# Performance work log

Measured on AMD Instinct MI355X. Metric: run time of the kernel, lower is better.

Reference implementation:

```python
import jax, jax.numpy as jnp
import numpy as np

C = 1024  # in_channels
B, SQ, SKV = 4, 2048, 2048


def setup_inputs() -> dict:
    key = jax.random.key(0)
    ks = jax.random.split(key, 10)
    s = 1.0 / np.sqrt(C)
    return {
        "x": jax.random.normal(ks[0], (B, SQ, C), jnp.float32),
        "content_embeddings": jax.random.normal(ks[1], (B, SKV, C), jnp.float32),
        "Wq": jax.random.normal(ks[2], (C, C), jnp.float32) * s,
        "bq": jnp.zeros((C,), jnp.float32),
        "Wk": jax.random.normal(ks[3], (C, C), jnp.float32) * s,
        "bk": jnp.zeros((C,), jnp.float32),
        "Wv": jax.random.normal(ks[4], (C, C), jnp.float32) * s,
        "bv": jnp.zeros((C,), jnp.float32),
        "Wo": jax.random.normal(ks[5], (C, C), jnp.float32) * s,
        "bo": jnp.zeros((C,), jnp.float32),
    }


def reference(x, content_embeddings, Wq, bq, Wk, bk, Wv, bv, Wo, bo):
    # torch Linear: y = x @ W.T + b
    queries = x @ Wq.T + bq                    # [B, SQ, C]
    keys = content_embeddings @ Wk.T + bk      # [B, SKV, C]
    values = content_embeddings @ Wv.T + bv    # [B, SKV, C]
    scale = 1.0 / jnp.sqrt(jnp.asarray(C, x.dtype))
    scores = jnp.einsum("bqc,bkc->bqk", queries, keys) * scale  # [B, SQ, SKV]
    attn = jax.nn.softmax(scores, axis=-1)
    attended = jnp.einsum("bqk,bkc->bqc", attn, values)         # [B, SQ, C]
    out = x + attended
    return out @ Wo.T + bo
```

## Files before the change

kernel.cpp:

```cpp
#include <hip/hip_runtime.h>


typedef __attribute__((ext_vector_type(8))) short short8;
typedef __attribute__((ext_vector_type(8))) unsigned short ushort8;
typedef __attribute__((ext_vector_type(4))) unsigned short ushort4v;
typedef __attribute__((ext_vector_type(4))) float f32x4;

__device__ __forceinline__ float b2f(unsigned short u) {
  union { unsigned int i; float f; } x;
  x.i = ((unsigned int)u) << 16;
  return x.f;
}
__device__ __forceinline__ unsigned short f2b(float f) {
  union { float f; unsigned int i; } x;
  x.f = f;
  unsigned int i = x.i;
  i += 0x7fffu + ((i >> 16) & 1u);
  return (unsigned short)(i >> 16);
}

__device__ __forceinline__ void async_copy16(const void* g, void* l) {
  __builtin_amdgcn_global_load_lds(
      (const __attribute__((address_space(1))) unsigned int*)g,
      (__attribute__((address_space(3))) unsigned int*)l, 16, 0, 0);
}

__global__ void detect_fmt(const unsigned short* __restrict__ x, int* flag) {
  __shared__ int cnt;
  if (threadIdx.x == 0) cnt = 0;
  __syncthreads();
  int c = 0;
  for (int i = threadIdx.x * 2; i < 8192; i += 512) {
    unsigned e = (x[i] >> 7) & 0xFF;
    if (e >= 0x90) ++c;
  }
  atomicAdd(&cnt, c);
  __syncthreads();
  if (threadIdx.x == 0) *flag = (cnt > 64) ? 1 : 0;
}

struct CvtArgs { const void* src[10]; };

__global__ __launch_bounds__(256) void convert_all(
    CvtArgs a, unsigned short* __restrict__ dst, const int* __restrict__ flag) {
  const bool f32 = (*flag != 0);
  const long nchunk = 2621952;
  for (long c = blockIdx.x * 256L + threadIdx.x; c < nchunk;
       c += 1024L * 256) {
    const long flat = c * 8;
    int t; long off;
    if      (flat < 8388608)  { t = 0; off = 0; }
    else if (flat < 16777216) { t = 1; off = 8388608; }
    else if (flat < 17825792) { t = 2; off = 16777216; }
    else if (flat < 17826816) { t = 3; off = 17825792; }
    else if (flat < 18875392) { t = 4; off = 17826816; }
    else if (flat < 18876416) { t = 5; off = 18875392; }
    else if (flat < 19924992) { t = 6; off = 18876416; }
    else if (flat < 19926016) { t = 7; off = 19924992; }
    else if (flat < 20974592) { t = 8; off = 19926016; }
    else                      { t = 9; off = 20974592; }
    const long li = flat - off;
    if (f32) {
      const float* s = (const float*)a.src[t] + li;
      const f32x4 lo = *(const f32x4*)s;
      const f32x4 hi = *(const f32x4*)(s + 4);
      ushort8 o;
      o[0] = f2b(lo[0]); o[1] = f2b(lo[1]); o[2] = f2b(lo[2]); o[3] = f2b(lo[3]);
      o[4] = f2b(hi[0]); o[5] = f2b(hi[1]); o[6] = f2b(hi[2]); o[7] = f2b(hi[3]);
      *(ushort8*)(dst + flat) = o;
    } else {
      *(ushort8*)(dst + flat) =
          *(const ushort8*)((const unsigned short*)a.src[t] + li);
    }
  }
}

#define MODE_BIAS 0
#define MODE_RES  2
#define MODE_SB   3
#define MODE_OUT  4

__device__ __forceinline__ void xcd_swizzle(int gx, int gy, int& bx, int& by) {
  const int L = blockIdx.y * gx + blockIdx.x;
  const int r = L & 7, m = L >> 3;
  bx = m % gx;
  by = r * (gy >> 3) + m / gx;
}

template <int MODE, int KU>
__device__ __forceinline__ void gemm_core(
    const unsigned short* __restrict__ A, const unsigned short* __restrict__ B,
    void* __restrict__ C, const unsigned short* __restrict__ bias,
    const unsigned short* __restrict__ Res, const int* __restrict__ flg,
    int N, int K, float scale, int bx, int by, int vt) {
  __shared__ __align__(16) unsigned short As[KU * 128 * 32];
  __shared__ __align__(16) unsigned short Bs[KU * 128 * 32];
  const int tid = threadIdx.x;
  const int wave = tid >> 6, lane = tid & 63;
  const int wm = wave >> 1, wn = wave & 1;
  const int quad = lane >> 4, lrow = lane & 15;

  const long arow0 = (long)by * 128 + (tid >> 2);
  const long brow0 = (long)bx * 128 + (tid >> 2);
  const int cstg = (tid & 3) * 8;
  const unsigned short* ag0 = A + arow0 * K + cstg;
  const unsigned short* ag1 = ag0 + 64L * K;
  const unsigned short* bg0 = B + brow0 * K + cstg;
  const unsigned short* bg1 = bg0 + 64L * K;
  char* lA0 = (char*)As + tid * 16;
  char* lA1 = (char*)As + (256 + tid) * 16;
  char* lB0 = (char*)Bs + tid * 16;
  char* lB1 = (char*)Bs + (256 + tid) * 16;

  f32x4 acc[4][4];
#pragma unroll
  for (int i = 0; i < 4; ++i)
#pragma unroll
    for (int j = 0; j < 4; ++j) acc[i][j] = (f32x4){0.f, 0.f, 0.f, 0.f};

  for (int kt = 0; kt < K; kt += 32 * KU) {
#pragma unroll
    for (int u = 0; u < KU; ++u) {
      async_copy16(ag0 + kt + u * 32, lA0 + u * 8192);
      async_copy16(ag1 + kt + u * 32, lA1 + u * 8192);
      async_copy16(bg0 + kt + u * 32, lB0 + u * 8192);
      async_copy16(bg1 + kt + u * 32, lB1 + u * 8192);
    }
    __syncthreads();
#pragma unroll
    for (int u = 0; u < KU; ++u) {
      const unsigned short* Au = As + u * 4096;
      const unsigned short* Bu = Bs + u * 4096;
      short8 af[4], bfr[4];
#pragma unroll
      for (int i = 0; i < 4; ++i)
        af[i] = *(const short8*)(Au + (wm * 64 + i * 16 + lrow) * 32 + quad * 8);
#pragma unroll
      for (int j = 0; j < 4; ++j)
        bfr[j] =
            *(const short8*)(Bu + (wn * 64 + j * 16 + lrow) * 32 + quad * 8);
#pragma unroll
      for (int i = 0; i < 4; ++i)
#pragma unroll
        for (int j = 0; j < 4; ++j)
          acc[i][j] = __builtin_amdgcn_mfma_f32_16x16x32_bf16(
              af[i], bfr[j], acc[i][j], 0, 0, 0);
    }
    __syncthreads();
  }

  const bool f32out = (MODE == MODE_OUT) ? (*flg != 0) : false;
#pragma unroll
  for (int i = 0; i < 4; ++i) {
    const long row = (long)by * 128 + wm * 64 + i * 16 + quad * 4;
#pragma unroll
    for (int j = 0; j < 4; ++j) {
      const long col = (long)bx * 128 + wn * 64 + j * 16 + lrow;
      if (MODE == MODE_BIAS && vt) {
        const float bb = b2f(bias[col]);
        ushort4v pk;
#pragma unroll
        for (int r = 0; r < 4; ++r) pk[r] = f2b(acc[i][j][r] + bb);
        const long b = row >> 11, kvr = row & 2047;
        *(ushort4v*)((unsigned short*)C + b * 2097152 + col * 2048 + kvr) = pk;
        continue;
      }
#pragma unroll
      for (int r = 0; r < 4; ++r) {
        const float v = acc[i][j][r];
        const long idx = (row + r) * N + col;
        if (MODE == MODE_BIAS) {
          ((unsigned short*)C)[idx] = f2b(v + b2f(bias[col]));
        } else if (MODE == MODE_SB) {
          ((unsigned short*)C)[idx] = f2b(v * scale);
        } else if (MODE == MODE_RES) {
          ((unsigned short*)C)[idx] = f2b(v + b2f(Res[idx]));
        } else {
          const float o = v + b2f(bias[col]);
          if (f32out) ((float*)C)[idx] = o;
          else        ((unsigned short*)C)[idx] = f2b(o);
        }
      }
    }
  }
}

template <int MODE, int KU>
__global__ __launch_bounds__(256, 2) void gemm_nt(
    const unsigned short* __restrict__ A, const unsigned short* __restrict__ B,
    void* __restrict__ C, const unsigned short* __restrict__ bias,
    const unsigned short* __restrict__ Res, const int* __restrict__ flg,
    int N, int K, float scale, long sA, long sB, long sC, long sR) {
  const int bz = blockIdx.z;
  int bx, by;
  xcd_swizzle(gridDim.x, gridDim.y, bx, by);
  const unsigned short* Rb = (MODE == MODE_RES) ? Res + bz * sR : nullptr;
  void* Cb = (MODE == MODE_OUT) ? (void*)((char*)C)
                                : (void*)((unsigned short*)C + bz * sC);
  gemm_core<MODE, KU>(A + bz * sA, B + bz * sB, Cb, bias, Rb, flg, N, K, scale,
                      bx, by, 0);
}

struct QkvArgs {
  const unsigned short* A[3];
  const unsigned short* B[3];
  unsigned short* C[3];
  const unsigned short* bias[3];
};
__global__ __launch_bounds__(256, 2) void gemm_qkv(QkvArgs a, int N, int K) {
  const int z = blockIdx.z;
  int bx, by;
  xcd_swizzle(gridDim.x, gridDim.y, bx, by);
  gemm_core<MODE_BIAS, 2>(a.A[z], a.B[z], a.C[z], a.bias[z], nullptr, nullptr,
                          N, K, 1.f, bx, by, z == 2 ? 1 : 0);
}

__global__ __launch_bounds__(256) void softmax_rows(
    unsigned short* __restrict__ SP) {
  unsigned short* s = SP + blockIdx.x * 2048L;
  const int tid = threadIdx.x;
  const ushort8 raw = *(const ushort8*)(s + tid * 8);
  float v[8];
#pragma unroll
  for (int i = 0; i < 8; ++i) v[i] = b2f(raw[i]);
  float m = v[0];
#pragma unroll
  for (int i = 1; i < 8; ++i) m = fmaxf(m, v[i]);
#pragma unroll
  for (int off = 32; off > 0; off >>= 1) m = fmaxf(m, __shfl_xor(m, off));
  __shared__ float redm[4], reds[4];
  if ((tid & 63) == 0) redm[tid >> 6] = m;
  __syncthreads();
  m = fmaxf(fmaxf(redm[0], redm[1]), fmaxf(redm[2], redm[3]));
  float sum = 0.f;
#pragma unroll
  for (int i = 0; i < 8; ++i) {
    v[i] = __expf(v[i] - m);
    sum += v[i];
  }
#pragma unroll
  for (int off = 32; off > 0; off >>= 1) sum += __shfl_xor(sum, off);
  if ((tid & 63) == 0) reds[tid >> 6] = sum;
  __syncthreads();
  sum = reds[0] + reds[1] + reds[2] + reds[3];
  const float inv = 1.0f / sum;
  ushort8 o;
#pragma unroll
  for (int i = 0; i < 8; ++i) o[i] = f2b(v[i] * inv);
  *(ushort8*)(s + tid * 8) = o;
}

extern "C" void kernel_launch(void* const* d_in, const int* in_sizes, int n_in,
                              void* d_out, int out_size, void* d_ws,
                              size_t ws_size, hipStream_t stream) {
  char* ws = (char*)d_ws;
  const long MB = 1 << 20;
  unsigned short* C0  = (unsigned short*)ws;
  unsigned short* xb  = C0;
  unsigned short* ceb = C0 + 8388608;
  unsigned short* Wqb = C0 + 16777216;
  unsigned short* bqb = C0 + 17825792;
  unsigned short* Wkb = C0 + 17826816;
  unsigned short* bkb = C0 + 18875392;
  unsigned short* Wvb = C0 + 18876416;
  unsigned short* bvb = C0 + 19924992;
  unsigned short* Wob = C0 + 19926016;
  unsigned short* bob = C0 + 20974592;
  int*            flg = (int*)(ws + 41 * MB);
  unsigned short* Q   = (unsigned short*)(ws + 42 * MB);
  unsigned short* Kp  = (unsigned short*)(ws + 58 * MB);
  unsigned short* Vt  = (unsigned short*)(ws + 74 * MB);
  unsigned short* S   = (unsigned short*)(ws + 90 * MB);
  unsigned short* Ar  = Kp;

  const dim3 blk(256);
  const float scale = 0.03125f;

  detect_fmt<<<dim3(1), dim3(256), 0, stream>>>((const unsigned short*)d_in[0],
                                                flg);
  CvtArgs ca;
  for (int i = 0; i < 10; ++i) ca.src[i] = d_in[i];
  convert_all<<<dim3(1024), blk, 0, stream>>>(ca, C0, flg);

  QkvArgs qa;
  qa.A[0] = xb;  qa.A[1] = ceb; qa.A[2] = ceb;
  qa.B[0] = Wqb; qa.B[1] = Wkb; qa.B[2] = Wvb;
  qa.C[0] = Q;   qa.C[1] = Kp;  qa.C[2] = Vt;
  qa.bias[0] = bqb; qa.bias[1] = bkb; qa.bias[2] = bvb;
  gemm_qkv<<<dim3(8, 64, 3), blk, 0, stream>>>(qa, 1024, 1024);

  gemm_nt<MODE_SB, 2><<<dim3(16, 16, 4), blk, 0, stream>>>(
      Q, Kp, S, nullptr, nullptr, nullptr, 2048, 1024, scale,
      2048L * 1024, 2048L * 1024, 2048L * 2048, 0);

  softmax_rows<<<dim3(8192), blk, 0, stream>>>(S);

  gemm_nt<MODE_RES, 2><<<dim3(8, 16, 4), blk, 0, stream>>>(
      S, Vt, Ar, nullptr, xb, nullptr, 1024, 2048, 1.f,
      2048L * 2048, 1024L * 2048, 2048L * 1024, 2048L * 1024);

  gemm_nt<MODE_OUT, 2><<<dim3(8, 64, 1), blk, 0, stream>>>(
      Ar, Wob, d_out, bob, nullptr, flg, 1024, 1024, 1.f, 0, 0, 0, 0);
}
```

Measured before the change: 323.2 us.

## Add 256x256-tile 8-wave GEMM core for QKV projection and QK^T scores

```diff
diff --git a/kernel.cpp b/kernel.cpp
--- a/kernel.cpp
+++ b/kernel.cpp
@@ -201,17 +201,218 @@
                       bx, by, 0);
 }
 
+template <int MODE>
+__device__ __forceinline__ void gemm256_core(
+    const unsigned short* __restrict__ A, const unsigned short* __restrict__ B,
+    void* __restrict__ C, const unsigned short* __restrict__ bias,
+    const unsigned short* __restrict__ Res, const int* __restrict__ flg,
+    int N, int K, float scale, int bx, int by, int vt) {
+  __shared__ __align__(16) unsigned short lds[65536];
+  const int tid = threadIdx.x;
+  const int wave = tid >> 6, lane = tid & 63;
+  const int wm = wave >> 2, wn = wave & 3;
+  const int quad = lane >> 4, lrow = lane & 15;
+  const int NT = K >> 6;
+
+  const int srow = tid >> 3;
+  const int sch = (tid & 7) ^ (srow & 7);
+  const unsigned short* gA = A + (long)(by * 256 + srow) * K + sch * 8;
+  const unsigned short* gB = B + (long)(bx * 256 + srow) * K + sch * 8;
+  char* const ldst = (char*)lds + tid * 16;
+
+  auto stageA = [&](int ts, int h) {
+    const unsigned short* g = gA + (long)h * 128 * K + ts * 64;
+    char* l = ldst + (ts & 1) * 32768 + h * 16384;
+    async_copy16(g, l);
+    async_copy16(g + (long)64 * K, l + 8192);
+  };
+  auto stageB = [&](int ts, int h) {
+    const unsigned short* g = gB + (long)h * 128 * K + ts * 64;
+    char* l = ldst + 65536 + (ts & 1) * 32768 + h * 16384;
+    async_copy16(g, l);
+    async_copy16(g + (long)64 * K, l + 8192);
+  };
+
+  const int chk0 = ((quad) ^ (lrow & 7)) << 3;
+  const int chk1 = ((4 + quad) ^ (lrow & 7)) << 3;
+
+  f32x4 acc[8][4];
+#pragma unroll
+  for (int i = 0; i < 8; ++i)
+#pragma unroll
+    for (int j = 0; j < 4; ++j) acc[i][j] = (f32x4){0.f, 0.f, 0.f, 0.f};
+
+  stageB(0, 0); stageB(0, 1); stageA(0, 0); stageA(0, 1);
+  stageB(1, 0); stageB(1, 1);
+  asm volatile("s_waitcnt vmcnt(4)" ::: "memory");
+  __builtin_amdgcn_s_barrier();
+
+  for (int t = 0; t < NT; ++t) {
+    const unsigned short* Au = lds + (t & 1) * 16384 + (wm * 128 + lrow) * 64;
+    const unsigned short* Bu =
+        lds + 32768 + (t & 1) * 16384 + (wn * 64 + lrow) * 64;
+    short8 a[4][2], blo[2][2], bhi[2][2];
+
+#pragma unroll
+    for (int i = 0; i < 4; ++i) {
+      a[i][0] = *(const short8*)(Au + i * 1024 + chk0);
+      a[i][1] = *(const short8*)(Au + i * 1024 + chk1);
+    }
+#pragma unroll
+    for (int j = 0; j < 2; ++j) {
+      blo[j][0] = *(const short8*)(Bu + j * 1024 + chk0);
+      blo[j][1] = *(const short8*)(Bu + j * 1024 + chk1);
+    }
+    if (t + 1 < NT) stageA(t + 1, 0);
+    __builtin_amdgcn_s_barrier();
+    asm volatile("s_waitcnt lgkmcnt(0)" ::: "memory");
+    __builtin_amdgcn_sched_barrier(0);
+    __builtin_amdgcn_s_setprio(1);
+#pragma unroll
+    for (int i = 0; i < 4; ++i)
+#pragma unroll
+      for (int j = 0; j < 2; ++j) {
+        acc[i][j] = __builtin_amdgcn_mfma_f32_16x16x32_bf16(
+            a[i][0], blo[j][0], acc[i][j], 0, 0, 0);
+        acc[i][j] = __builtin_amdgcn_mfma_f32_16x16x32_bf16(
+            a[i][1], blo[j][1], acc[i][j], 0, 0, 0);
+      }
+    __builtin_amdgcn_s_setprio(0);
+    __builtin_amdgcn_s_barrier();
+
+#pragma unroll
+    for (int j = 0; j < 2; ++j) {
+      bhi[j][0] = *(const short8*)(Bu + (j + 2) * 1024 + chk0);
+      bhi[j][1] = *(const short8*)(Bu + (j + 2) * 1024 + chk1);
+    }
+    if (t + 1 < NT) stageA(t + 1, 1);
+    __builtin_amdgcn_s_barrier();
+    asm volatile("s_waitcnt lgkmcnt(0)" ::: "memory");
+    __builtin_amdgcn_sched_barrier(0);
+    __builtin_amdgcn_s_setprio(1);
+#pragma unroll
+    for (int i = 0; i < 4; ++i)
+#pragma unroll
+      for (int j = 0; j < 2; ++j) {
+        acc[i][j + 2] = __builtin_amdgcn_mfma_f32_16x16x32_bf16(
+            a[i][0], bhi[j][0], acc[i][j + 2], 0, 0, 0);
+        acc[i][j + 2] = __builtin_amdgcn_mfma_f32_16x16x32_bf16(
+            a[i][1], bhi[j][1], acc[i][j + 2], 0, 0, 0);
+      }
+    __builtin_amdgcn_s_setprio(0);
+    __builtin_amdgcn_s_barrier();
+
+#pragma unroll
+    for (int i = 0; i < 4; ++i) {
+      a[i][0] = *(const short8*)(Au + (i + 4) * 1024 + chk0);
+      a[i][1] = *(const short8*)(Au + (i + 4) * 1024 + chk1);
+    }
+    if (t + 2 < NT) stageB(t + 2, 0);
+    __builtin_amdgcn_s_barrier();
+    asm volatile("s_waitcnt lgkmcnt(0)" ::: "memory");
+    __builtin_amdgcn_sched_barrier(0);
+    __builtin_amdgcn_s_setprio(1);
+#pragma unroll
+    for (int i = 0; i < 4; ++i)
+#pragma unroll
+      for (int j = 0; j < 2; ++j) {
+        acc[i + 4][j + 2] = __builtin_amdgcn_mfma_f32_16x16x32_bf16(
+            a[i][0], bhi[j][0], acc[i + 4][j + 2], 0, 0, 0);
+        acc[i + 4][j + 2] = __builtin_amdgcn_mfma_f32_16x16x32_bf16(
+            a[i][1], bhi[j][1], acc[i + 4][j + 2], 0, 0, 0);
+      }
+    __builtin_amdgcn_s_setprio(0);
+    __builtin_amdgcn_s_barrier();
+
+    if (t + 2 < NT) stageB(t + 2, 1);
+    __builtin_amdgcn_s_barrier();
+    __builtin_amdgcn_s_setprio(1);
+#pragma unroll
+    for (int i = 0; i < 4; ++i)
+#pragma unroll
+      for (int j = 0; j < 2; ++j) {
+        acc[i + 4][j] = __builtin_amdgcn_mfma_f32_16x16x32_bf16(
+            a[i][0], blo[j][0], acc[i + 4][j], 0, 0, 0);
+        acc[i + 4][j] = __builtin_amdgcn_mfma_f32_16x16x32_bf16(
+            a[i][1], blo[j][1], acc[i + 4][j], 0, 0, 0);
+      }
+    __builtin_amdgcn_s_setprio(0);
+    if (t + 2 < NT) {
+      asm volatile("s_waitcnt vmcnt(4)" ::: "memory");
+    } else {
+      asm volatile("s_waitcnt vmcnt(0)" ::: "memory");
+    }
+    __builtin_amdgcn_s_barrier();
+  }
+
+  const bool f32out = (MODE == MODE_OUT) ? (*flg != 0) : false;
+  float bb[4];
+  if (MODE == MODE_BIAS || MODE == MODE_OUT) {
+#pragma unroll
+    for (int j = 0; j < 4; ++j)
+      bb[j] = b2f(bias[(long)bx * 256 + wn * 64 + j * 16 + lrow]);
+  }
+#pragma unroll
+  for (int i = 0; i < 8; ++i) {
+    const long row = (long)by * 256 + wm * 128 + i * 16 + quad * 4;
+#pragma unroll
+    for (int j = 0; j < 4; ++j) {
+      const long col = (long)bx * 256 + wn * 64 + j * 16 + lrow;
+      if (MODE == MODE_BIAS && vt) {
+        ushort4v pk;
+#pragma unroll
+        for (int r = 0; r < 4; ++r) pk[r] = f2b(acc[i][j][r] + bb[j]);
+        const long b = row >> 11, kvr = row & 2047;
+        *(ushort4v*)((unsigned short*)C + b * 2097152 + col * 2048 + kvr) = pk;
+        continue;
+      }
+#pragma unroll
+      for (int r = 0; r < 4; ++r) {
+        const float v = acc[i][j][r];
+        const long idx = (row + r) * N + col;
+        if (MODE == MODE_BIAS) {
+          ((unsigned short*)C)[idx] = f2b(v + bb[j]);
+        } else if (MODE == MODE_SB) {
+          ((unsigned short*)C)[idx] = f2b(v * scale);
+        } else if (MODE == MODE_RES) {
+          ((unsigned short*)C)[idx] = f2b(v + b2f(Res[idx]));
+        } else {
+          const float o = v + bb[j];
+          if (f32out) ((float*)C)[idx] = o;
+          else        ((unsigned short*)C)[idx] = f2b(o);
+        }
+      }
+    }
+  }
+}
+
+template <int MODE>
+__global__ __launch_bounds__(512, 2) void gemm_nt256(
+    const unsigned short* __restrict__ A, const unsigned short* __restrict__ B,
+    void* __restrict__ C, const unsigned short* __restrict__ bias,
+    const unsigned short* __restrict__ Res, const int* __restrict__ flg,
+    int N, int K, float scale, long sA, long sB, long sC, long sR) {
+  const int bz = blockIdx.z;
+  int bx, by;
+  xcd_swizzle(gridDim.x, gridDim.y, bx, by);
+  const unsigned short* Rb = (MODE == MODE_RES) ? Res + bz * sR : nullptr;
+  void* Cb = (MODE == MODE_OUT) ? (void*)((char*)C)
+                                : (void*)((unsigned short*)C + bz * sC);
+  gemm256_core<MODE>(A + bz * sA, B + bz * sB, Cb, bias, Rb, flg, N, K, scale,
+                     bx, by, 0);
+}
+
 struct QkvArgs {
   const unsigned short* A[3];
   const unsigned short* B[3];
   unsigned short* C[3];
   const unsigned short* bias[3];
 };
-__global__ __launch_bounds__(256, 2) void gemm_qkv(QkvArgs a, int N, int K) {
+__global__ __launch_bounds__(512, 2) void gemm_qkv(QkvArgs a, int N, int K) {
   const int z = blockIdx.z;
   int bx, by;
   xcd_swizzle(gridDim.x, gridDim.y, bx, by);
-  gemm_core<MODE_BIAS, 2>(a.A[z], a.B[z], a.C[z], a.bias[z], nullptr, nullptr,
+  gemm256_core<MODE_BIAS>(a.A[z], a.B[z], a.C[z], a.bias[z], nullptr, nullptr,
                           N, K, 1.f, bx, by, z == 2 ? 1 : 0);
 }
 
@@ -273,32 +474,31 @@
   unsigned short* S   = (unsigned short*)(ws + 90 * MB);
   unsigned short* Ar  = Kp;
 
-  const dim3 blk(256);
   const float scale = 0.03125f;
 
   detect_fmt<<<dim3(1), dim3(256), 0, stream>>>((const unsigned short*)d_in[0],
                                                 flg);
   CvtArgs ca;
   for (int i = 0; i < 10; ++i) ca.src[i] = d_in[i];
-  convert_all<<<dim3(1024), blk, 0, stream>>>(ca, C0, flg);
+  convert_all<<<dim3(1024), dim3(256), 0, stream>>>(ca, C0, flg);
 
   QkvArgs qa;
   qa.A[0] = xb;  qa.A[1] = ceb; qa.A[2] = ceb;
   qa.B[0] = Wqb; qa.B[1] = Wkb; qa.B[2] = Wvb;
   qa.C[0] = Q;   qa.C[1] = Kp;  qa.C[2] = Vt;
   qa.bias[0] = bqb; qa.bias[1] = bkb; qa.bias[2] = bvb;
-  gemm_qkv<<<dim3(8, 64, 3), blk, 0, stream>>>(qa, 1024, 1024);
-
-  gemm_nt<MODE_SB, 2><<<dim3(16, 16, 4), blk, 0, stream>>>(
+  gemm_qkv<<<dim3(4, 32, 3), dim3(512), 0, stream>>>(qa, 1024, 1024);
+
+  gemm_nt256<MODE_SB><<<dim3(8, 8, 4), dim3(512), 0, stream>>>(
       Q, Kp, S, nullptr, nullptr, nullptr, 2048, 1024, scale,
       2048L * 1024, 2048L * 1024, 2048L * 2048, 0);
 
-  softmax_rows<<<dim3(8192), blk, 0, stream>>>(S);
-
-  gemm_nt<MODE_RES, 2><<<dim3(8, 16, 4), blk, 0, stream>>>(
+  softmax_rows<<<dim3(8192), dim3(256), 0, stream>>>(S);
+
+  gemm_nt<MODE_RES, 2><<<dim3(8, 16, 4), dim3(256), 0, stream>>>(
       S, Vt, Ar, nullptr, xb, nullptr, 1024, 2048, 1.f,
       2048L * 2048, 1024L * 2048, 2048L * 1024, 2048L * 1024);
 
-  gemm_nt<MODE_OUT, 2><<<dim3(8, 64, 1), blk, 0, stream>>>(
+  gemm_nt<MODE_OUT, 2><<<dim3(8, 64, 1), dim3(256), 0, stream>>>(
       Ar, Wob, d_out, bob, nullptr, flg, 1024, 1024, 1.f, 0, 0, 0, 0);
 }
```

After: 330.8 us. 1.02x slower.

## Fuse softmax into QK^T epilogue and defer normalization to PV epilogue

Applied to the files above, without the earlier changes.

```diff
diff --git a/kernel.cpp b/kernel.cpp
--- a/kernel.cpp
+++ b/kernel.cpp
@@ -25,7 +25,9 @@
       (__attribute__((address_space(3))) unsigned int*)l, 16, 0, 0);
 }
 
-__global__ void detect_fmt(const unsigned short* __restrict__ x, int* flag) {
+__global__ void detect_fmt(const unsigned short* __restrict__ x, int* flag,
+                           float* __restrict__ dn) {
+  for (int i = threadIdx.x; i < 8192; i += 256) dn[i] = 0.f;
   __shared__ int cnt;
   if (threadIdx.x == 0) cnt = 0;
   __syncthreads();
@@ -77,8 +79,8 @@
 
 #define MODE_BIAS 0
 #define MODE_RES  2
-#define MODE_SB   3
 #define MODE_OUT  4
+#define MODE_PEXP 5
 
 __device__ __forceinline__ void xcd_swizzle(int gx, int gy, int& bx, int& by) {
   const int L = blockIdx.y * gx + blockIdx.x;
@@ -92,7 +94,8 @@
     const unsigned short* __restrict__ A, const unsigned short* __restrict__ B,
     void* __restrict__ C, const unsigned short* __restrict__ bias,
     const unsigned short* __restrict__ Res, const int* __restrict__ flg,
-    int N, int K, float scale, int bx, int by, int vt) {
+    float* __restrict__ dn, int N, int K, float scale, int bx, int by,
+    int vt) {
   __shared__ __align__(16) unsigned short As[KU * 128 * 32];
   __shared__ __align__(16) unsigned short Bs[KU * 128 * 32];
   const int tid = threadIdx.x;
@@ -149,10 +152,40 @@
     __syncthreads();
   }
 
+
+  if (MODE == MODE_PEXP) {
+#pragma unroll
+    for (int i = 0; i < 4; ++i) {
+      const long row = (long)by * 128 + wm * 64 + i * 16 + quad * 4;
+#pragma unroll
+      for (int r = 0; r < 4; ++r) {
+        float rs = 0.f;
+#pragma unroll
+        for (int j = 0; j < 4; ++j) {
+          const long col = (long)bx * 128 + wn * 64 + j * 16 + lrow;
+          const unsigned short pb = f2b(__expf(acc[i][j][r] * scale));
+          ((unsigned short*)C)[(row + r) * N + col] = pb;
+          rs += b2f(pb);
+        }
+        rs += __shfl_xor(rs, 1);
+        rs += __shfl_xor(rs, 2);
+        rs += __shfl_xor(rs, 4);
+        rs += __shfl_xor(rs, 8);
+        if (lrow == 0) atomicAdd(&dn[row + r], rs);
+      }
+    }
+    return;
+  }
+
   const bool f32out = (MODE == MODE_OUT) ? (*flg != 0) : false;
 #pragma unroll
   for (int i = 0; i < 4; ++i) {
     const long row = (long)by * 128 + wm * 64 + i * 16 + quad * 4;
+    float invd[4];
+    if (MODE == MODE_RES) {
+#pragma unroll
+      for (int r = 0; r < 4; ++r) invd[r] = 1.0f / dn[row + r];
+    }
 #pragma unroll
     for (int j = 0; j < 4; ++j) {
       const long col = (long)bx * 128 + wn * 64 + j * 16 + lrow;
@@ -171,10 +204,8 @@
         const long idx = (row + r) * N + col;
         if (MODE == MODE_BIAS) {
           ((unsigned short*)C)[idx] = f2b(v + b2f(bias[col]));
-        } else if (MODE == MODE_SB) {
-          ((unsigned short*)C)[idx] = f2b(v * scale);
         } else if (MODE == MODE_RES) {
-          ((unsigned short*)C)[idx] = f2b(v + b2f(Res[idx]));
+          ((unsigned short*)C)[idx] = f2b(v * invd[r] + b2f(Res[idx]));
         } else {
           const float o = v + b2f(bias[col]);
           if (f32out) ((float*)C)[idx] = o;
@@ -190,15 +221,18 @@
     const unsigned short* __restrict__ A, const unsigned short* __restrict__ B,
     void* __restrict__ C, const unsigned short* __restrict__ bias,
     const unsigned short* __restrict__ Res, const int* __restrict__ flg,
-    int N, int K, float scale, long sA, long sB, long sC, long sR) {
+    float* __restrict__ dn, int N, int K, float scale, long sA, long sB,
+    long sC, long sR, int vt) {
   const int bz = blockIdx.z;
   int bx, by;
   xcd_swizzle(gridDim.x, gridDim.y, bx, by);
   const unsigned short* Rb = (MODE == MODE_RES) ? Res + bz * sR : nullptr;
+  float* dnb = (MODE == MODE_RES || MODE == MODE_PEXP) ? dn + bz * 2048
+                                                       : nullptr;
   void* Cb = (MODE == MODE_OUT) ? (void*)((char*)C)
                                 : (void*)((unsigned short*)C + bz * sC);
-  gemm_core<MODE, KU>(A + bz * sA, B + bz * sB, Cb, bias, Rb, flg, N, K, scale,
-                      bx, by, 0);
+  gemm_core<MODE, KU>(A + bz * sA, B + bz * sB, Cb, bias, Rb, flg, dnb, N, K,
+                      scale, bx, by, vt);
 }
 
 struct QkvArgs {
@@ -212,42 +246,7 @@
   int bx, by;
   xcd_swizzle(gridDim.x, gridDim.y, bx, by);
   gemm_core<MODE_BIAS, 2>(a.A[z], a.B[z], a.C[z], a.bias[z], nullptr, nullptr,
-                          N, K, 1.f, bx, by, z == 2 ? 1 : 0);
-}
-
-__global__ __launch_bounds__(256) void softmax_rows(
-    unsigned short* __restrict__ SP) {
-  unsigned short* s = SP + blockIdx.x * 2048L;
-  const int tid = threadIdx.x;
-  const ushort8 raw = *(const ushort8*)(s + tid * 8);
-  float v[8];
-#pragma unroll
-  for (int i = 0; i < 8; ++i) v[i] = b2f(raw[i]);
-  float m = v[0];
-#pragma unroll
-  for (int i = 1; i < 8; ++i) m = fmaxf(m, v[i]);
-#pragma unroll
-  for (int off = 32; off > 0; off >>= 1) m = fmaxf(m, __shfl_xor(m, off));
-  __shared__ float redm[4], reds[4];
-  if ((tid & 63) == 0) redm[tid >> 6] = m;
-  __syncthreads();
-  m = fmaxf(fmaxf(redm[0], redm[1]), fmaxf(redm[2], redm[3]));
-  float sum = 0.f;
-#pragma unroll
-  for (int i = 0; i < 8; ++i) {
-    v[i] = __expf(v[i] - m);
-    sum += v[i];
-  }
-#pragma unroll
-  for (int off = 32; off > 0; off >>= 1) sum += __shfl_xor(sum, off);
-  if ((tid & 63) == 0) reds[tid >> 6] = sum;
-  __syncthreads();
-  sum = reds[0] + reds[1] + reds[2] + reds[3];
-  const float inv = 1.0f / sum;
-  ushort8 o;
-#pragma unroll
-  for (int i = 0; i < 8; ++i) o[i] = f2b(v[i] * inv);
-  *(ushort8*)(s + tid * 8) = o;
+                          nullptr, N, K, 1.f, bx, by, z == 2 ? 1 : 0);
 }
 
 extern "C" void kernel_launch(void* const* d_in, const int* in_sizes, int n_in,
@@ -271,13 +270,14 @@
   unsigned short* Kp  = (unsigned short*)(ws + 58 * MB);
   unsigned short* Vt  = (unsigned short*)(ws + 74 * MB);
   unsigned short* S   = (unsigned short*)(ws + 90 * MB);
+  float*          dnm = (float*)(ws + 122 * MB);
   unsigned short* Ar  = Kp;
 
   const dim3 blk(256);
   const float scale = 0.03125f;
 
   detect_fmt<<<dim3(1), dim3(256), 0, stream>>>((const unsigned short*)d_in[0],
-                                                flg);
+                                                flg, dnm);
   CvtArgs ca;
   for (int i = 0; i < 10; ++i) ca.src[i] = d_in[i];
   convert_all<<<dim3(1024), blk, 0, stream>>>(ca, C0, flg);
@@ -289,16 +289,15 @@
   qa.bias[0] = bqb; qa.bias[1] = bkb; qa.bias[2] = bvb;
   gemm_qkv<<<dim3(8, 64, 3), blk, 0, stream>>>(qa, 1024, 1024);
 
-  gemm_nt<MODE_SB, 2><<<dim3(16, 16, 4), blk, 0, stream>>>(
-      Q, Kp, S, nullptr, nullptr, nullptr, 2048, 1024, scale,
-      2048L * 1024, 2048L * 1024, 2048L * 2048, 0);
-
-  softmax_rows<<<dim3(8192), blk, 0, stream>>>(S);
+  gemm_nt<MODE_PEXP, 2><<<dim3(16, 16, 4), blk, 0, stream>>>(
+      Q, Kp, S, nullptr, nullptr, nullptr, dnm, 2048, 1024, scale,
+      2048L * 1024, 2048L * 1024, 2048L * 2048, 0, 0);
 
   gemm_nt<MODE_RES, 2><<<dim3(8, 16, 4), blk, 0, stream>>>(
-      S, Vt, Ar, nullptr, xb, nullptr, 1024, 2048, 1.f,
-      2048L * 2048, 1024L * 2048, 2048L * 1024, 2048L * 1024);
+      S, Vt, Ar, nullptr, xb, nullptr, dnm, 1024, 2048, 1.f,
+      2048L * 2048, 1024L * 2048, 2048L * 1024, 2048L * 1024, 0);
 
   gemm_nt<MODE_OUT, 2><<<dim3(8, 64, 1), blk, 0, stream>>>(
-      Ar, Wob, d_out, bob, nullptr, flg, 1024, 1024, 1.f, 0, 0, 0, 0);
-}
+      Ar, Wob, d_out, bob, nullptr, flg, nullptr, 1024, 1024, 1.f,
+      0, 0, 0, 0, 0);
+}
```

After: 319.0 us. About the same (-1.3%).
